# Optimization experiments

Hardware: AMD Instinct MI355X
Metric: run time of the kernel (lower is better)

Reference implementation:

```python
import jax, jax.numpy as jnp
import numpy as np

VOCAB = 32000
EMB = 256
HID = 512
SEQ = 512
SOS = 1  # word2vec key_to_index['<SOS>']; PAD assumed index 0 and never sampled


def setup_inputs() -> dict:
    key = jax.random.key(0)
    ks = jax.random.split(key, 8)
    k_lstm = 1.0 / np.sqrt(HID)
    k_out = 1.0 / np.sqrt(HID)
    return {
        # token ids in [2, VOCAB) so the PAD-skip branch never triggers
        "input_seq": jax.random.randint(ks[0], (1, SEQ), 2, VOCAB, dtype=jnp.int32),
        "h0": jnp.zeros((1, 1, HID), jnp.float32),
        "c0": jnp.zeros((1, 1, HID), jnp.float32),
        "embedding": jax.random.normal(ks[1], (VOCAB, EMB), jnp.float32) * 0.02,
        "W_ih": jax.random.uniform(ks[2], (4 * HID, EMB), jnp.float32, -k_lstm, k_lstm),
        "W_hh": jax.random.uniform(ks[3], (4 * HID, HID), jnp.float32, -k_lstm, k_lstm),
        "b_ih": jax.random.uniform(ks[4], (4 * HID,), jnp.float32, -k_lstm, k_lstm),
        "b_hh": jax.random.uniform(ks[5], (4 * HID,), jnp.float32, -k_lstm, k_lstm),
        "W_out": jax.random.uniform(ks[6], (VOCAB, HID), jnp.float32, -k_out, k_out),
        "b_out": jax.random.uniform(ks[7], (VOCAB,), jnp.float32, -k_out, k_out),
    }


def reference(input_seq, h0, c0, embedding, W_ih, W_hh, b_ih, b_hh, W_out, b_out):
    # tokens actually fed to the LSTM: <SOS> then the full teacher-forced sequence
    tokens = jnp.concatenate([jnp.array([SOS], jnp.int32), input_seq[0]])  # [S+1]
    emb = embedding[tokens]  # [S+1, E]
    bias = b_ih + b_hh

    def cell(carry, x_t):
        h, c = carry  # [H], [H]
        gates = W_ih @ x_t + W_hh @ h + bias  # [4H], torch gate order i,f,g,o
        i, f, g, o = jnp.split(gates, 4)
        i = jax.nn.sigmoid(i)
        f = jax.nn.sigmoid(f)
        g = jnp.tanh(g)
        o = jax.nn.sigmoid(o)
        c_new = f * c + i * g
        h_new = o * jnp.tanh(c_new)
        return (h_new, c_new), h_new

    (hT, cT), hs = jax.lax.scan(cell, (h0[0, 0], c0[0, 0]), emb)  # hs: [S+1, H]
    logits = hs @ W_out.T + b_out  # [S+1, V] (same math as per-step Linear + cat)
    outputs = logits[None]  # [1, S+1, V]
    return outputs, hT[None, None], cT[None, None]
```

## Files before the change

### kernel.cpp

```cpp
#include <hip/hip_runtime.h>
#include <cmath>

#define VOCAB 32000
#define EMB   256
#define HID   512
#define TLEN  513
#define G4    2048
#define NWG   32
#define SOS   1
#define NPRE  264
#define NCVT  4000

typedef unsigned long long u64;
typedef unsigned int uivec4 __attribute__((ext_vector_type(4)));
typedef float f32x4 __attribute__((ext_vector_type(4)));
typedef short bf16x8 __attribute__((ext_vector_type(8)));

__device__ inline float fsig(float x)  { return __builtin_amdgcn_rcpf(1.f + __expf(-x)); }
__device__ inline float ftanh(float x) { return 1.f - 2.f * __builtin_amdgcn_rcpf(__expf(2.f * x) + 1.f); }
__device__ inline float fma4(f32x4 w, f32x4 h, float a) {
    return fmaf(w[0], h[0], fmaf(w[1], h[1], fmaf(w[2], h[2], fmaf(w[3], h[3], a))));
}

__device__ inline void bf16split(float f, short& h, short& l) {
    unsigned u = __float_as_uint(f);
    unsigned r = u + (0x7fffu + ((u >> 16) & 1u));
    unsigned hb = r & 0xffff0000u;
    h = (short)(hb >> 16);
    float res = f - __uint_as_float(hb);
    unsigned u2 = __float_as_uint(res);
    unsigned r2 = u2 + (0x7fffu + ((u2 >> 16) & 1u));
    l = (short)(r2 >> 16);
}

__global__ __launch_bounds__(256) void pre_fused(
    const int* __restrict__ seq, const float* __restrict__ emb,
    const float* __restrict__ W_ih, const float* __restrict__ b_ih,
    const float* __restrict__ b_hh, const float* __restrict__ W_out,
    float* __restrict__ Xg, u64* pk,
    short* __restrict__ Wh, short* __restrict__ Wl, int do_split)
{
    __shared__ __align__(16) float ebuf[16][EMB];
    const int b   = blockIdx.x;
    const int tid = threadIdx.x;

    if (b >= NPRE) {
        if (!do_split) return;
        if (b == NPRE) {
#pragma unroll
            for (int i = 0; i < 4; ++i) pk[tid + 256 * i] = 0;
        }
        const size_t base = (size_t)(b - NPRE) * 4096 + (size_t)tid * 16;
        const float4* src = (const float4*)(W_out + base);
        float4 f0 = src[0], f1 = src[1], f2 = src[2], f3 = src[3];
        float fv[16] = { f0.x,f0.y,f0.z,f0.w, f1.x,f1.y,f1.z,f1.w,
                         f2.x,f2.y,f2.z,f2.w, f3.x,f3.y,f3.z,f3.w };
        union { short s[8]; bf16x8 v; } h0_, h1_, l0_, l1_;
#pragma unroll
        for (int e = 0; e < 8; ++e) bf16split(fv[e],     h0_.s[e], l0_.s[e]);
#pragma unroll
        for (int e = 0; e < 8; ++e) bf16split(fv[8 + e], h1_.s[e], l1_.s[e]);
        *(bf16x8*)&Wh[base]     = h0_.v;
        *(bf16x8*)&Wh[base + 8] = h1_.v;
        *(bf16x8*)&Wl[base]     = l0_.v;
        *(bf16x8*)&Wl[base + 8] = l1_.v;
        return;
    }

    const int bt = b % 33;
    const int br = b / 33;

    for (int tt = 0; tt < 16; ++tt) {
        int t = bt * 16 + tt;
        if (t < TLEN) {
            int tok = (t == 0) ? SOS : seq[t - 1];
            ebuf[tt][tid] = emb[(size_t)tok * EMB + tid];
        }
    }
    __syncthreads();

    const int row = br * 256 + tid;
    float acc[16];
#pragma unroll
    for (int tt = 0; tt < 16; ++tt) acc[tt] = 0.f;

    const float4* wp = (const float4*)(W_ih + (size_t)row * EMB);
#pragma unroll 4
    for (int k4 = 0; k4 < EMB / 4; ++k4) {
        float4 w = wp[k4];
#pragma unroll
        for (int tt = 0; tt < 16; ++tt) {
            float4 e = *(const float4*)&ebuf[tt][k4 * 4];
            acc[tt] = fmaf(w.x, e.x, fmaf(w.y, e.y, fmaf(w.z, e.z, fmaf(w.w, e.w, acc[tt]))));
        }
    }

    const float bias = b_ih[row] + b_hh[row];
    for (int tt = 0; tt < 16; ++tt) {
        int t = bt * 16 + tt;
        if (t < TLEN) Xg[(size_t)t * G4 + row] = acc[tt] + bias;
    }
}

__global__ __launch_bounds__(256, 1) void lstm_recurrence(
    const float* __restrict__ Xg, const float* __restrict__ W_hh,
    const float* __restrict__ h0, const float* __restrict__ c0,
    float* __restrict__ hs, short* __restrict__ hs_h, short* __restrict__ hs_l,
    u64* pk, float* __restrict__ out_hT, float* __restrict__ out_cT)
{
    __shared__ __align__(16) float hbuf[HID];
    __shared__ float pbuf[2][256];

    const int wg  = blockIdx.x;
    const int tid = threadIdx.x;
    const int wv  = tid >> 6;
    const int ln  = tid & 63;
    const int q   = ln >> 4;
    const int j   = ln & 15;
    const int row = q * HID + wg * 16 + j;

    f32x4 wreg[32];
    const f32x4* wp = (const f32x4*)(W_hh + (size_t)row * HID + wv * 128);
#pragma unroll
    for (int i = 0; i < 32; ++i) wreg[i] = wp[i];

    float c = (tid < 16) ? c0[wg * 16 + tid] : 0.f;
    {
        float2 h2 = *(const float2*)&h0[tid * 2];
        hbuf[tid * 2]     = h2.x;
        hbuf[tid * 2 + 1] = h2.y;
    }
    __syncthreads();

    for (int t = 0; t < TLEN; ++t) {
        float xg0 = 0.f, xg1 = 0.f, xg2 = 0.f, xg3 = 0.f;
        if (tid < 16) {
            const float* xp = Xg + (size_t)t * G4 + wg * 16 + tid;
            xg0 = xp[0]; xg1 = xp[512]; xg2 = xp[1024]; xg3 = xp[1536];
        }

        if (t > 0) {
            const unsigned tt = (unsigned)t;
            u64 sa = (u64)(uintptr_t)(pk + (size_t)(t & 1) * HID + 2 * tid);
            uivec4 r;
            do {
                asm volatile("global_load_dwordx4 %0, %1, off sc0 sc1\n\t"
                             "s_waitcnt vmcnt(0)" : "=v"(r) : "v"(sa));
            } while (r.y != tt || r.w != tt);
            hbuf[2 * tid]     = __uint_as_float(r.x);
            hbuf[2 * tid + 1] = __uint_as_float(r.z);
            asm volatile("s_waitcnt lgkmcnt(0)" ::: "memory");
        }

        float a0 = 0.f, a1 = 0.f, a2 = 0.f, a3 = 0.f;
        float a4 = 0.f, a5 = 0.f, a6 = 0.f, a7 = 0.f;
        const f32x4* hp = (const f32x4*)&hbuf[wv * 128];
#pragma unroll
        for (int i = 0; i < 32; i += 8) {
            a0 = fma4(wreg[i],     hp[i],     a0);
            a1 = fma4(wreg[i + 1], hp[i + 1], a1);
            a2 = fma4(wreg[i + 2], hp[i + 2], a2);
            a3 = fma4(wreg[i + 3], hp[i + 3], a3);
            a4 = fma4(wreg[i + 4], hp[i + 4], a4);
            a5 = fma4(wreg[i + 5], hp[i + 5], a5);
            a6 = fma4(wreg[i + 6], hp[i + 6], a6);
            a7 = fma4(wreg[i + 7], hp[i + 7], a7);
        }
        pbuf[t & 1][tid] = ((a0 + a1) + (a2 + a3)) + ((a4 + a5) + (a6 + a7));
        __syncthreads();

        if (tid < 16) {
            const float* pb = pbuf[t & 1];
            float gi = pb[tid]      + pb[64 + tid]  + pb[128 + tid] + pb[192 + tid] + xg0;
            float gf = pb[16 + tid] + pb[80 + tid]  + pb[144 + tid] + pb[208 + tid] + xg1;
            float gg = pb[32 + tid] + pb[96 + tid]  + pb[160 + tid] + pb[224 + tid] + xg2;
            float go = pb[48 + tid] + pb[112 + tid] + pb[176 + tid] + pb[240 + tid] + xg3;
            float i_ = fsig(gi);
            float f_ = fsig(gf);
            float g_ = ftanh(gg);
            float o_ = fsig(go);
            c = fmaf(f_, c, i_ * g_);
            float h_ = o_ * ftanh(c);
            if (t < TLEN - 1) {
                u64 word = ((u64)(unsigned)(t + 1) << 32) | (u64)__float_as_uint(h_);
                (void)__hip_atomic_exchange(
                    &pk[(size_t)((t + 1) & 1) * HID + wg * 16 + tid], word,
                    __ATOMIC_RELAXED, __HIP_MEMORY_SCOPE_AGENT);
            } else {
                out_hT[wg * 16 + tid] = h_;
                out_cT[wg * 16 + tid] = c;
            }
            hs[(size_t)t * HID + wg * 16 + tid] = h_;
            short hh, hl; bf16split(h_, hh, hl);
            hs_h[(size_t)t * HID + wg * 16 + tid] = hh;
            hs_l[(size_t)t * HID + wg * 16 + tid] = hl;
        }
    }
}

#define GLDT 40

__global__ __launch_bounds__(256, 2) void out_gemm_pre(
    const short* __restrict__ hs_h, const short* __restrict__ hs_l,
    const short* __restrict__ Wh, const short* __restrict__ Wl,
    const float* __restrict__ b_out, float* __restrict__ out)
{
    __shared__ __align__(16) short Ah[128][GLDT];
    __shared__ __align__(16) short Al[128][GLDT];
    __shared__ __align__(16) short Bh[128][GLDT];
    __shared__ __align__(16) short Bl[128][GLDT];

    const int tb = blockIdx.x;
    const int vb = blockIdx.y;
    const int tid = threadIdx.x;
    const int w   = tid >> 6;
    const int l   = tid & 63;
    const int l15 = l & 15;
    const int lg  = l >> 4;
    const int m0 = tb * 128, n0 = vb * 128;

    const int sr = tid >> 1;
    const int kh = (tid & 1) * 16;

    f32x4 acc[2][8];
#pragma unroll
    for (int s = 0; s < 2; ++s)
#pragma unroll
        for (int cc = 0; cc < 8; ++cc) acc[s][cc] = (f32x4){0.f, 0.f, 0.f, 0.f};

    for (int k0 = 0; k0 < HID; k0 += 32) {
        {
            int trow = m0 + sr;
            bf16x8 z = (bf16x8)(short)0;
            bf16x8 ah0 = z, ah1 = z, al0 = z, al1 = z;
            if (trow < TLEN) {
                const size_t o = (size_t)trow * HID + k0 + kh;
                ah0 = *(const bf16x8*)&hs_h[o];
                ah1 = *(const bf16x8*)&hs_h[o + 8];
                al0 = *(const bf16x8*)&hs_l[o];
                al1 = *(const bf16x8*)&hs_l[o + 8];
            }
            *(bf16x8*)&Ah[sr][kh]     = ah0;
            *(bf16x8*)&Ah[sr][kh + 8] = ah1;
            *(bf16x8*)&Al[sr][kh]     = al0;
            *(bf16x8*)&Al[sr][kh + 8] = al1;
        }
        {
            const size_t o = (size_t)(n0 + sr) * HID + k0 + kh;
            *(bf16x8*)&Bh[sr][kh]     = *(const bf16x8*)&Wh[o];
            *(bf16x8*)&Bh[sr][kh + 8] = *(const bf16x8*)&Wh[o + 8];
            *(bf16x8*)&Bl[sr][kh]     = *(const bf16x8*)&Wl[o];
            *(bf16x8*)&Bl[sr][kh + 8] = *(const bf16x8*)&Wl[o + 8];
        }
        __syncthreads();

        bf16x8 ah[2], al2[2];
#pragma unroll
        for (int s = 0; s < 2; ++s) {
            ah[s]  = *(const bf16x8*)&Ah[32 * w + 16 * s + l15][8 * lg];
            al2[s] = *(const bf16x8*)&Al[32 * w + 16 * s + l15][8 * lg];
        }
#pragma unroll
        for (int cc = 0; cc < 8; ++cc) {
            bf16x8 bh = *(const bf16x8*)&Bh[16 * cc + l15][8 * lg];
            bf16x8 bl = *(const bf16x8*)&Bl[16 * cc + l15][8 * lg];
#pragma unroll
            for (int s = 0; s < 2; ++s) {
                acc[s][cc] = __builtin_amdgcn_mfma_f32_16x16x32_bf16(ah[s],  bh, acc[s][cc], 0, 0, 0);
                acc[s][cc] = __builtin_amdgcn_mfma_f32_16x16x32_bf16(ah[s],  bl, acc[s][cc], 0, 0, 0);
                acc[s][cc] = __builtin_amdgcn_mfma_f32_16x16x32_bf16(al2[s], bh, acc[s][cc], 0, 0, 0);
            }
        }
        __syncthreads();
    }

#pragma unroll
    for (int cc = 0; cc < 8; ++cc) {
        int col = n0 + 16 * cc + l15;
        float bo = b_out[col];
#pragma unroll
        for (int s = 0; s < 2; ++s) {
            int rbase = m0 + 32 * w + 16 * s + lg * 4;
#pragma unroll
            for (int r = 0; r < 4; ++r) {
                int trow = rbase + r;
                if (trow < TLEN) out[(size_t)trow * VOCAB + col] = acc[s][cc][r] + bo;
            }
        }
    }
}

__global__ __launch_bounds__(256, 2) void out_gemm_mfma(
    const float* __restrict__ hs, const float* __restrict__ W_out,
    const float* __restrict__ b_out, float* __restrict__ out)
{
    __shared__ __align__(16) short Ah[128][GLDT];
    __shared__ __align__(16) short Al[128][GLDT];
    __shared__ __align__(16) short Bh[128][GLDT];
    __shared__ __align__(16) short Bl[128][GLDT];

    const int tb = blockIdx.x;
    const int vb = blockIdx.y;
    const int tid = threadIdx.x;
    const int w   = tid >> 6;
    const int l   = tid & 63;
    const int l15 = l & 15;
    const int lg  = l >> 4;
    const int m0 = tb * 128, n0 = vb * 128;

    const int sr = tid >> 1;
    const int kh = (tid & 1) * 16;

    f32x4 acc[2][8];
#pragma unroll
    for (int s = 0; s < 2; ++s)
#pragma unroll
        for (int cc = 0; cc < 8; ++cc) acc[s][cc] = (f32x4){0.f, 0.f, 0.f, 0.f};

    for (int k0 = 0; k0 < HID; k0 += 32) {
        {
            int trow = m0 + sr;
            float4 fa0 = make_float4(0.f,0.f,0.f,0.f), fa1 = fa0, fa2 = fa0, fa3 = fa0;
            if (trow < TLEN) {
                const float4* ap = (const float4*)(hs + (size_t)trow * HID + k0 + kh);
                fa0 = ap[0]; fa1 = ap[1]; fa2 = ap[2]; fa3 = ap[3];
            }
            float fv[16] = { fa0.x,fa0.y,fa0.z,fa0.w, fa1.x,fa1.y,fa1.z,fa1.w,
                             fa2.x,fa2.y,fa2.z,fa2.w, fa3.x,fa3.y,fa3.z,fa3.w };
#pragma unroll
            for (int g = 0; g < 2; ++g) {
                union { short s[8]; bf16x8 v; } ph, pl;
#pragma unroll
                for (int e = 0; e < 8; ++e) bf16split(fv[g * 8 + e], ph.s[e], pl.s[e]);
                *(bf16x8*)&Ah[sr][kh + 8 * g] = ph.v;
                *(bf16x8*)&Al[sr][kh + 8 * g] = pl.v;
            }
        }
        {
            const float4* bp = (const float4*)(W_out + (size_t)(n0 + sr) * HID + k0 + kh);
            float4 fb0 = bp[0], fb1 = bp[1], fb2 = bp[2], fb3 = bp[3];
            float fv[16] = { fb0.x,fb0.y,fb0.z,fb0.w, fb1.x,fb1.y,fb1.z,fb1.w,
                             fb2.x,fb2.y,fb2.z,fb2.w, fb3.x,fb3.y,fb3.z,fb3.w };
#pragma unroll
            for (int g = 0; g < 2; ++g) {
                union { short s[8]; bf16x8 v; } ph, pl;
#pragma unroll
                for (int e = 0; e < 8; ++e) bf16split(fv[g * 8 + e], ph.s[e], pl.s[e]);
                *(bf16x8*)&Bh[sr][kh + 8 * g] = ph.v;
                *(bf16x8*)&Bl[sr][kh + 8 * g] = pl.v;
            }
        }
        __syncthreads();

        bf16x8 ah[2], al2[2];
#pragma unroll
        for (int s = 0; s < 2; ++s) {
            ah[s]  = *(const bf16x8*)&Ah[32 * w + 16 * s + l15][8 * lg];
            al2[s] = *(const bf16x8*)&Al[32 * w + 16 * s + l15][8 * lg];
        }
#pragma unroll
        for (int cc = 0; cc < 8; ++cc) {
            bf16x8 bh = *(const bf16x8*)&Bh[16 * cc + l15][8 * lg];
            bf16x8 bl = *(const bf16x8*)&Bl[16 * cc + l15][8 * lg];
#pragma unroll
            for (int s = 0; s < 2; ++s) {
                acc[s][cc] = __builtin_amdgcn_mfma_f32_16x16x32_bf16(ah[s],  bh, acc[s][cc], 0, 0, 0);
                acc[s][cc] = __builtin_amdgcn_mfma_f32_16x16x32_bf16(ah[s],  bl, acc[s][cc], 0, 0, 0);
                acc[s][cc] = __builtin_amdgcn_mfma_f32_16x16x32_bf16(al2[s], bh, acc[s][cc], 0, 0, 0);
            }
        }
        __syncthreads();
    }

#pragma unroll
    for (int cc = 0; cc < 8; ++cc) {
        int col = n0 + 16 * cc + l15;
        float bo = b_out[col];
#pragma unroll
        for (int s = 0; s < 2; ++s) {
            int rbase = m0 + 32 * w + 16 * s + lg * 4;
#pragma unroll
            for (int r = 0; r < 4; ++r) {
                int trow = rbase + r;
                if (trow < TLEN) out[(size_t)trow * VOCAB + col] = acc[s][cc][r] + bo;
            }
        }
    }
}

extern "C" void kernel_launch(void* const* d_in, const int* in_sizes, int n_in,
                              void* d_out, int out_size, void* d_ws, size_t ws_size,
                              hipStream_t stream)
{
    const int*   seq   = (const int*)  d_in[0];
    const float* h0    = (const float*)d_in[1];
    const float* c0    = (const float*)d_in[2];
    const float* emb   = (const float*)d_in[3];
    const float* W_ih  = (const float*)d_in[4];
    const float* W_hh  = (const float*)d_in[5];
    const float* b_ih  = (const float*)d_in[6];
    const float* b_hh  = (const float*)d_in[7];
    const float* W_out = (const float*)d_in[8];
    const float* b_out = (const float*)d_in[9];

    float* out_logits = (float*)d_out;
    float* out_hT     = out_logits + (size_t)TLEN * VOCAB;
    float* out_cT     = out_hT + HID;

    char*  base = (char*)d_ws;
    float* Xg   = (float*)base;
    float* hs   = (float*)(base + 4202496);
    u64*   pk   = (u64*)  (base + 4202496 + 1050624);
    short* hs_h = (short*)(base + 5261312);
    short* hs_l = (short*)(base + 5261312 + 525312);
    short* Wh   = (short*)(base + 6311936);
    short* Wl   = (short*)(base + 6311936 + 32768000);
    const size_t need_pre = 6311936ull + 2ull * 32768000ull;

    const int use_pre = (ws_size >= need_pre) ? 1 : 0;

    if (use_pre) {
        pre_fused<<<NPRE + NCVT, 256, 0, stream>>>(seq, emb, W_ih, b_ih, b_hh, W_out,
                                                   Xg, pk, Wh, Wl, 1);
        lstm_recurrence<<<NWG, 256, 0, stream>>>(Xg, W_hh, h0, c0, hs, hs_h, hs_l, pk,
                                                 out_hT, out_cT);
        out_gemm_pre<<<dim3(5, 250), 256, 0, stream>>>(hs_h, hs_l, Wh, Wl, b_out, out_logits);
    } else {
        (void)hipMemsetAsync(pk, 0, 2 * HID * sizeof(u64), stream);
        pre_fused<<<NPRE, 256, 0, stream>>>(seq, emb, W_ih, b_ih, b_hh, W_out,
                                            Xg, pk, hs_h , hs_l , 0);
        lstm_recurrence<<<NWG, 256, 0, stream>>>(Xg, W_hh, h0, c0, hs, hs_h, hs_l, pk,
                                                 out_hT, out_cT);
        out_gemm_mfma<<<dim3(5, 250), 256, 0, stream>>>(hs, W_out, b_out, out_logits);
    }
}
```

Before: 981.5 us.

## Overlap W_out bf16 split conversion with LSTM recurrence using extra blocks

Moves the W_out hi/lo bf16 split conversion out of the pre-gate kernel and into extra workgroups launched alongside the 32 recurrence workgroups. Those 224 blocks grid-stride over W_out while the latency-bound recurrence runs on a few CUs, so the conversion cost is hidden. The gate precompute kernel becomes a 2D grid and also zeroes the sync flags. The risk is that the conversion blocks compete with the recurrence for memory bandwidth and L2, or delay residency of the recurrence blocks if they are scheduled first, which matters because those blocks spin-wait on each other.

```diff
diff --git a/kernel.cpp b/kernel.cpp
--- a/kernel.cpp
+++ b/kernel.cpp
@@ -7,9 +7,10 @@
 #define TLEN  513
 #define G4    2048
 #define NWG   32
+#define NCONV 224
 #define SOS   1
 #define NPRE  264
-#define NCVT  4000
+#define WOUT_ELEMS 16384000ull
 
 typedef unsigned long long u64;
 typedef unsigned int uivec4 __attribute__((ext_vector_type(4)));
@@ -33,42 +34,20 @@
     l = (short)(r2 >> 16);
 }
 
-__global__ __launch_bounds__(256) void pre_fused(
+__global__ __launch_bounds__(256) void precompute_gates(
     const int* __restrict__ seq, const float* __restrict__ emb,
     const float* __restrict__ W_ih, const float* __restrict__ b_ih,
-    const float* __restrict__ b_hh, const float* __restrict__ W_out,
-    float* __restrict__ Xg, u64* pk,
-    short* __restrict__ Wh, short* __restrict__ Wl, int do_split)
+    const float* __restrict__ b_hh, float* __restrict__ Xg, u64* pk)
 {
     __shared__ __align__(16) float ebuf[16][EMB];
-    const int b   = blockIdx.x;
+    const int bt = blockIdx.x;
+    const int br = blockIdx.y;
     const int tid = threadIdx.x;
 
-    if (b >= NPRE) {
-        if (!do_split) return;
-        if (b == NPRE) {
-#pragma unroll
-            for (int i = 0; i < 4; ++i) pk[tid + 256 * i] = 0;
-        }
-        const size_t base = (size_t)(b - NPRE) * 4096 + (size_t)tid * 16;
-        const float4* src = (const float4*)(W_out + base);
-        float4 f0 = src[0], f1 = src[1], f2 = src[2], f3 = src[3];
-        float fv[16] = { f0.x,f0.y,f0.z,f0.w, f1.x,f1.y,f1.z,f1.w,
-                         f2.x,f2.y,f2.z,f2.w, f3.x,f3.y,f3.z,f3.w };
-        union { short s[8]; bf16x8 v; } h0_, h1_, l0_, l1_;
-#pragma unroll
-        for (int e = 0; e < 8; ++e) bf16split(fv[e],     h0_.s[e], l0_.s[e]);
-#pragma unroll
-        for (int e = 0; e < 8; ++e) bf16split(fv[8 + e], h1_.s[e], l1_.s[e]);
-        *(bf16x8*)&Wh[base]     = h0_.v;
-        *(bf16x8*)&Wh[base + 8] = h1_.v;
-        *(bf16x8*)&Wl[base]     = l0_.v;
-        *(bf16x8*)&Wl[base + 8] = l1_.v;
-        return;
-    }
-
-    const int bt = b % 33;
-    const int br = b / 33;
+    if (bt == 0 && br == 0) {
+#pragma unroll
+        for (int i = 0; i < 4; ++i) pk[tid + 256 * i] = 0;
+    }
 
     for (int tt = 0; tt < 16; ++tt) {
         int t = bt * 16 + tt;
@@ -105,14 +84,38 @@
 __global__ __launch_bounds__(256, 1) void lstm_recurrence(
     const float* __restrict__ Xg, const float* __restrict__ W_hh,
     const float* __restrict__ h0, const float* __restrict__ c0,
+    const float* __restrict__ W_out, short* __restrict__ Wh, short* __restrict__ Wl,
     float* __restrict__ hs, short* __restrict__ hs_h, short* __restrict__ hs_l,
-    u64* pk, float* __restrict__ out_hT, float* __restrict__ out_cT)
+    u64* pk, float* __restrict__ out_hT, float* __restrict__ out_cT, int do_conv)
 {
     __shared__ __align__(16) float hbuf[HID];
     __shared__ float pbuf[2][256];
 
+    const int tid = threadIdx.x;
+
+    if (blockIdx.x >= NWG) {
+        if (!do_conv) return;
+        const int cb = blockIdx.x - NWG;
+        const size_t stride = (size_t)NCONV * 256 * 16;
+        for (size_t i = ((size_t)cb * 256 + tid) * 16; i < WOUT_ELEMS; i += stride) {
+            const float4* src = (const float4*)(W_out + i);
+            float4 f0 = src[0], f1 = src[1], f2 = src[2], f3 = src[3];
+            float fv[16] = { f0.x,f0.y,f0.z,f0.w, f1.x,f1.y,f1.z,f1.w,
+                             f2.x,f2.y,f2.z,f2.w, f3.x,f3.y,f3.z,f3.w };
+            union { short s[8]; bf16x8 v; } h0_, h1_, l0_, l1_;
+#pragma unroll
+            for (int e = 0; e < 8; ++e) bf16split(fv[e],     h0_.s[e], l0_.s[e]);
+#pragma unroll
+            for (int e = 0; e < 8; ++e) bf16split(fv[8 + e], h1_.s[e], l1_.s[e]);
+            *(bf16x8*)&Wh[i]     = h0_.v;
+            *(bf16x8*)&Wh[i + 8] = h1_.v;
+            *(bf16x8*)&Wl[i]     = l0_.v;
+            *(bf16x8*)&Wl[i + 8] = l1_.v;
+        }
+        return;
+    }
+
     const int wg  = blockIdx.x;
-    const int tid = threadIdx.x;
     const int wv  = tid >> 6;
     const int ln  = tid & 63;
     const int q   = ln >> 4;
@@ -419,18 +422,14 @@
 
     const int use_pre = (ws_size >= need_pre) ? 1 : 0;
 
+    precompute_gates<<<dim3(33, 8), 256, 0, stream>>>(seq, emb, W_ih, b_ih, b_hh, Xg, pk);
     if (use_pre) {
-        pre_fused<<<NPRE + NCVT, 256, 0, stream>>>(seq, emb, W_ih, b_ih, b_hh, W_out,
-                                                   Xg, pk, Wh, Wl, 1);
-        lstm_recurrence<<<NWG, 256, 0, stream>>>(Xg, W_hh, h0, c0, hs, hs_h, hs_l, pk,
-                                                 out_hT, out_cT);
+        lstm_recurrence<<<NWG + NCONV, 256, 0, stream>>>(
+            Xg, W_hh, h0, c0, W_out, Wh, Wl, hs, hs_h, hs_l, pk, out_hT, out_cT, 1);
         out_gemm_pre<<<dim3(5, 250), 256, 0, stream>>>(hs_h, hs_l, Wh, Wl, b_out, out_logits);
     } else {
-        (void)hipMemsetAsync(pk, 0, 2 * HID * sizeof(u64), stream);
-        pre_fused<<<NPRE, 256, 0, stream>>>(seq, emb, W_ih, b_ih, b_hh, W_out,
-                                            Xg, pk, hs_h , hs_l , 0);
-        lstm_recurrence<<<NWG, 256, 0, stream>>>(Xg, W_hh, h0, c0, hs, hs_h, hs_l, pk,
-                                                 out_hT, out_cT);
+        lstm_recurrence<<<NWG, 256, 0, stream>>>(
+            Xg, W_hh, h0, c0, W_out, Wh, Wl, hs, hs_h, hs_l, pk, out_hT, out_cT, 0);
         out_gemm_mfma<<<dim3(5, 250), 256, 0, stream>>>(hs, W_out, b_out, out_logits);
     }
 }
```

Result: no change. 968.0 us (-1.4%).
